# Performance work log

Measured on AMD Instinct MI355X. Metric: run time of the kernel, lower is better.

Reference implementation:

```python
import jax, jax.numpy as jnp
import numpy as np

B, S, D = 4, 2048, 1024
H, DK, DV = 16, 64, 64
SCALE = 8.0  # scaling_factor = sqrt(dk)


def setup_inputs() -> dict:
    key = jax.random.key(0)
    ks = jax.random.split(key, 9)
    s = 1.0 / np.sqrt(D)
    return {
        "q": jax.random.normal(ks[0], (B, S, D), jnp.float32),
        "k": jax.random.normal(ks[1], (B, S, D), jnp.float32),
        "v": jax.random.normal(ks[2], (B, S, D), jnp.float32),
        "Wq": jax.random.uniform(ks[3], (D, H * DK), jnp.float32, -s, s),
        "bq": jax.random.uniform(ks[4], (H * DK,), jnp.float32, -s, s),
        "Wk": jax.random.uniform(ks[5], (D, H * DK), jnp.float32, -s, s),
        "bk": jax.random.uniform(ks[6], (H * DK,), jnp.float32, -s, s),
        "Wv": jax.random.uniform(ks[7], (D, H * DV), jnp.float32, -s, s),
        "bv": jax.random.uniform(ks[8], (H * DV,), jnp.float32, -s, s),
    }


def reference(q, k, v, Wq, bq, Wk, bk, Wv, bv):
    # Linear projections, then split heads: [B,S,H*d] -> [B,S,H,d]
    qh = (q @ Wq + bq).reshape(B, S, H, DK)
    kh = (k @ Wk + bk).reshape(B, S, H, DK)
    vh = (v @ Wv + bv).reshape(B, S, H, DV)
    # scores: [B,H,Sq,Sk]
    e = jnp.einsum("bqhd,bkhd->bhqk", qh, kh) / SCALE
    attn = jax.nn.softmax(e, axis=-1)
    out = jnp.einsum("bhqk,bkhd->bqhd", attn, vh)  # [B,Sq,H,DV]
    return out.reshape(B, S, H * DV)  # dropout p=0 -> identity
```

## Files before the change

kernel.cpp:

```cpp
#include <hip/hip_runtime.h>
#include <hip/hip_bf16.h>


typedef unsigned short u16;
typedef unsigned int   u32;
typedef short bf16x8 __attribute__((ext_vector_type(8)));
typedef short bf16x4 __attribute__((ext_vector_type(4)));
typedef float f32x4  __attribute__((ext_vector_type(4)));
typedef u32   u32x4  __attribute__((ext_vector_type(4)));

#define S_TOT 2048
#define HD    1024
#define QK_SCALE 0.18033688f

#if __has_builtin(__builtin_amdgcn_exp2f)
#define EXP2(x) __builtin_amdgcn_exp2f(x)
#else
#define EXP2(x) exp2f(x)
#endif

__device__ __forceinline__ u16 f2bf(float f) {
  union { float f; unsigned u; } v; v.f = f;
  unsigned r = v.u + 0x7FFFu + ((v.u >> 16) & 1u);
  return (u16)(r >> 16);
}

__device__ __forceinline__ u32 cvt_pk_bf16(float lo, float hi) {
  u32 r;
  asm("v_cvt_pk_bf16_f32 %0, %1, %2" : "=v"(r) : "v"(lo), "v"(hi));
  return r;
}

__device__ __forceinline__ bf16x4 ds_tr16(unsigned a) {
  bf16x4 d;
  asm volatile("ds_read_b64_tr_b16 %0, %1" : "=v"(d) : "v"(a) : "memory");
  return d;
}

__device__ __forceinline__ void gld16(const u16* g, u16* l) {
  __builtin_amdgcn_global_load_lds(
      (const __attribute__((address_space(1))) u32*)g,
      (__attribute__((address_space(3))) u32*)l, 16, 0, 0);
}

#define LGKM_FENCE() do { asm volatile("s_waitcnt lgkmcnt(0)" ::: "memory"); \
                          __builtin_amdgcn_sched_barrier(0); } while (0)

#define PIPE_BAR(N) do { asm volatile("s_waitcnt vmcnt(" #N ")" ::: "memory"); \
                         __builtin_amdgcn_s_barrier(); \
                         __builtin_amdgcn_sched_barrier(0); } while (0)

__global__ __launch_bounds__(256)
void conv_kernel(const float* __restrict__ x0, const float* __restrict__ x1, const float* __restrict__ x2,
                 const float* __restrict__ w0, const float* __restrict__ w1, const float* __restrict__ w2,
                 u16* __restrict__ Xb, u16* __restrict__ Wt)
{
  const int z = blockIdx.y;
  const int t = threadIdx.x;
  if (blockIdx.x < 1024) {
    const float* X = z == 0 ? x0 : (z == 1 ? x1 : x2);
    u16* Xz = Xb + (size_t)z * 8388608;
    int tid = blockIdx.x * 256 + t;
#pragma unroll
    for (int i = 0; i < 8; ++i) {
      int c = tid + i * 262144;
      int row = c >> 8, k4 = (c & 255) * 4;
      const float4 xv = *(const float4*)&X[(size_t)row * 1024 + k4];
      int p = (k4 & ~31) + 8 * ((k4 & 15) >> 2) + 4 * ((k4 >> 4) & 1);
      p ^= (row & 6) << 2;
      bf16x4 sv = { (short)f2bf(xv.x), (short)f2bf(xv.y), (short)f2bf(xv.z), (short)f2bf(xv.w) };
      *(bf16x4*)&Xz[(size_t)row * 1024 + p] = sv;
    }
  } else {
    const float* W = z == 0 ? w0 : (z == 1 ? w1 : w2);
    u16* Wz = Wt + (size_t)z * 1048576;
    int tid = (blockIdx.x - 1024) * 256 + t;
#pragma unroll
    for (int i = 0; i < 8; ++i) {
      int c = tid + i * 32768;
      int n = c & 1023, k4 = (c >> 10) * 4;
      float wv0 = W[(size_t)(k4 + 0) * 1024 + n];
      float wv1 = W[(size_t)(k4 + 1) * 1024 + n];
      float wv2 = W[(size_t)(k4 + 2) * 1024 + n];
      float wv3 = W[(size_t)(k4 + 3) * 1024 + n];
      int kl = k4 & 31;
      int kp = 8 * ((kl & 15) >> 2) + 4 * ((kl >> 4) & 1);
      int off = ((n >> 7) * 32 + (k4 >> 5)) * 4096 + (n & 127) * 32
              + (kp ^ ((n & 6) << 2));
      bf16x4 sv = { (short)f2bf(wv0), (short)f2bf(wv1), (short)f2bf(wv2), (short)f2bf(wv3) };
      *(bf16x4*)&Wz[off] = sv;
    }
  }
}

__global__ __launch_bounds__(256)
void gemm_kernel(const u16* __restrict__ Xb, const u16* __restrict__ Wt,
                 const float* __restrict__ b0, const float* __restrict__ b1, const float* __restrict__ b2,
                 u16* __restrict__ o0, u16* __restrict__ o1, u16* __restrict__ vT)
{
  int p  = blockIdx.x + 8 * blockIdx.y + 512 * blockIdx.z;
  int wk = (p & 7) * 192 + (p >> 3);
  int nb = wk & 7, mb = (wk >> 3) & 63, z = wk >> 9;

  const u16* Xz = Xb + (size_t)z * 8388608;
  const u16* Wz = Wt + (size_t)z * 1048576;
  const float* BS = z == 0 ? b0 : (z == 1 ? b1 : b2);
  const float  osc = (z == 0) ? QK_SCALE : 1.0f;

  const int t = threadIdx.x;
  const int lane = t & 63, wid = t >> 6;
  const int g = lane >> 4, ln = lane & 15;
  const int mbase = mb * 128, nbase = nb * 128;
  const int xr = (ln & 6) << 2;

  __shared__ __align__(16) u16 Al[3][128 * 32];
  __shared__ __align__(16) u16 Bl[3][128 * 32];

  f32x4 acc[4][4];
#pragma unroll
  for (int i = 0; i < 4; ++i)
#pragma unroll
    for (int j = 0; j < 4; ++j) { acc[i][j][0]=0.f; acc[i][j][1]=0.f; acc[i][j][2]=0.f; acc[i][j][3]=0.f; }

  const u16* sa = Xz + (size_t)(mbase + (t >> 2)) * 1024 + (t & 3) * 8;
  const u16* sb = Wz + (size_t)(nb * 32) * 4096 + t * 8;
  u16* alw[3] = { &Al[0][wid * 512], &Al[1][wid * 512], &Al[2][wid * 512] };
  u16* blw[3] = { &Bl[0][wid * 512], &Bl[1][wid * 512], &Bl[2][wid * 512] };

  auto stage = [&](int kb, int buf) __attribute__((always_inline)) {
    gld16(sa + kb * 32,               alw[buf]);
    gld16(sa + kb * 32 + 64 * 1024,   alw[buf] + 2048);
    gld16(sb + kb * 4096,             blw[buf]);
    gld16(sb + kb * 4096 + 2048,      blw[buf] + 2048);
  };

  stage(0, 0);
  stage(1, 1);
  PIPE_BAR(4);

  if (z < 2) {
    const int wm = wid >> 1, wn = wid & 1;
    u16* O = z == 0 ? o0 : o1;

    auto compute = [&](int cur) __attribute__((always_inline)) {
      bf16x8 af[4], bfv[4];
#pragma unroll
      for (int mf = 0; mf < 4; ++mf)
        af[mf] = *(const bf16x8*)&Al[cur][(wm * 64 + mf * 16 + ln) * 32 + (g * 8 ^ xr)];
#pragma unroll
      for (int nf = 0; nf < 4; ++nf)
        bfv[nf] = *(const bf16x8*)&Bl[cur][(wn * 64 + nf * 16 + ln) * 32 + (g * 8 ^ xr)];
      __builtin_amdgcn_s_setprio(1);
#pragma unroll
      for (int mf = 0; mf < 4; ++mf)
#pragma unroll
        for (int nf = 0; nf < 4; ++nf)
          acc[mf][nf] = __builtin_amdgcn_mfma_f32_16x16x32_bf16(af[mf], bfv[nf], acc[mf][nf], 0, 0, 0);
      __builtin_amdgcn_s_setprio(0);
    };

    for (int kb = 0; kb < 30; kb += 3) {
      stage(kb + 2, 2); compute(0); PIPE_BAR(4);
      stage(kb + 3, 0); compute(1); PIPE_BAR(4);
      stage(kb + 4, 1); compute(2); PIPE_BAR(4);
    }
    compute(0); PIPE_BAR(0);
    compute(1);

#pragma unroll
    for (int nf = 0; nf < 4; ++nf) {
      int n = nbase + wn * 64 + nf * 16 + ln;
      float bv = BS[n];
#pragma unroll
      for (int mf = 0; mf < 4; ++mf)
#pragma unroll
        for (int r = 0; r < 4; ++r) {
          int m = mbase + wm * 64 + mf * 16 + 4 * g + r;
          O[(size_t)m * 1024 + n] = f2bf((acc[mf][nf][r] + bv) * osc);
        }
    }
  } else {
    const int wseq = wid >> 1, wdv = wid & 1;

    auto compute2 = [&](int cur) __attribute__((always_inline)) {
      bf16x8 afw[4], bfx[4];
#pragma unroll
      for (int mf = 0; mf < 4; ++mf)
        afw[mf] = *(const bf16x8*)&Bl[cur][(wdv * 64 + mf * 16 + ln) * 32 + (g * 8 ^ xr)];
#pragma unroll
      for (int nf = 0; nf < 4; ++nf)
        bfx[nf] = *(const bf16x8*)&Al[cur][(wseq * 64 + nf * 16 + ln) * 32 + (g * 8 ^ xr)];
      __builtin_amdgcn_s_setprio(1);
#pragma unroll
      for (int mf = 0; mf < 4; ++mf)
#pragma unroll
        for (int nf = 0; nf < 4; ++nf)
          acc[mf][nf] = __builtin_amdgcn_mfma_f32_16x16x32_bf16(afw[mf], bfx[nf], acc[mf][nf], 0, 0, 0);
      __builtin_amdgcn_s_setprio(0);
    };

    for (int kb = 0; kb < 30; kb += 3) {
      stage(kb + 2, 2); compute2(0); PIPE_BAR(4);
      stage(kb + 3, 0); compute2(1); PIPE_BAR(4);
      stage(kb + 4, 1); compute2(2); PIPE_BAR(4);
    }
    compute2(0); PIPE_BAR(0);
    compute2(1);

#pragma unroll
    for (int mf = 0; mf < 4; ++mf)
#pragma unroll
      for (int r = 0; r < 4; ++r) {
        int dvg = nbase + wdv * 64 + mf * 16 + 4 * g + r;
        float bv = BS[dvg];
        int hh = dvg >> 6, dvl = dvg & 63;
#pragma unroll
        for (int nf = 0; nf < 4; ++nf) {
          int m = mbase + wseq * 64 + nf * 16 + ln;
          int bb = m >> 11, ss = m & 2047;
          vT[((size_t)(bb * 16 + hh) * 64 + dvl) * 2048 + ss] = f2bf(acc[mf][nf][r] + bv);
        }
      }
  }
}

__global__ __launch_bounds__(256)
void proj_kernel(const float* __restrict__ x0, const float* __restrict__ x1, const float* __restrict__ x2,
                 const float* __restrict__ w0, const float* __restrict__ w1, const float* __restrict__ w2,
                 const float* __restrict__ b0, const float* __restrict__ b1, const float* __restrict__ b2,
                 u16* __restrict__ o0, u16* __restrict__ o1, u16* __restrict__ vT)
{
  int p  = blockIdx.x + 8 * blockIdx.y + 512 * blockIdx.z;
  int wk = (p & 7) * 192 + (p >> 3);
  int nb = wk & 7, mb = (wk >> 3) & 63, z = wk >> 9;

  const float* X  = z == 0 ? x0 : (z == 1 ? x1 : x2);
  const float* W  = z == 0 ? w0 : (z == 1 ? w1 : w2);
  const float* BS = z == 0 ? b0 : (z == 1 ? b1 : b2);
  const float  osc = (z == 0) ? QK_SCALE : 1.0f;

  const int t = threadIdx.x;
  const int lane = t & 63, wid = t >> 6;
  const int g = lane >> 4, ln = lane & 15;
  const int wm = wid >> 1, wn = wid & 1;
  const int mbase = mb * 128, nbase = nb * 128;

  __shared__ __align__(16) u16 As[128 * 40];
  __shared__ __align__(16) u16 Bs[16 * 272];

  f32x4 acc[4][4];
#pragma unroll
  for (int i = 0; i < 4; ++i)
#pragma unroll
    for (int j = 0; j < 4; ++j) { acc[i][j][0]=0.f; acc[i][j][1]=0.f; acc[i][j][2]=0.f; acc[i][j][3]=0.f; }

  const int arow = t >> 3;
  const int ak0  = (t & 7) * 4;
  const int ap   = 8 * ((ak0 & 15) >> 2) + 4 * (ak0 >> 4);
  const int bkr  = t >> 5;
  const int bnc  = (t & 31) * 4;
  const int bnblk = bnc >> 4, bncl = bnc & 15;

  const unsigned bs_base = (unsigned)(size_t)&Bs[0];

  for (int kb = 0; kb < 32; ++kb) {
    const int kbase = kb * 32;
#pragma unroll
    for (int ps = 0; ps < 4; ++ps) {
      int row = arow + 32 * ps;
      const float4 xv = *(const float4*)&X[(size_t)(mbase + row) * 1024 + kbase + ak0];
      bf16x4 sv = { (short)f2bf(xv.x), (short)f2bf(xv.y), (short)f2bf(xv.z), (short)f2bf(xv.w) };
      *(bf16x4*)&As[row * 40 + ap] = sv;
    }
#pragma unroll
    for (int ps = 0; ps < 4; ++ps) {
      int kr = bkr + 8 * ps;
      const float4 wv = *(const float4*)&W[(size_t)(kbase + kr) * 1024 + nbase + bnc];
      bf16x4 sv = { (short)f2bf(wv.x), (short)f2bf(wv.y), (short)f2bf(wv.z), (short)f2bf(wv.w) };
      *(bf16x4*)&Bs[(bnblk * 2 + (kr >> 4)) * 272 + (kr & 15) * 16 + bncl] = sv;
    }
    __syncthreads();

    bf16x8 af[4];
#pragma unroll
    for (int mf = 0; mf < 4; ++mf)
      af[mf] = *(const bf16x8*)&As[(wm * 64 + mf * 16 + ln) * 40 + g * 8];

    bf16x8 bfv[4];
#pragma unroll
    for (int nf = 0; nf < 4; ++nf) {
      unsigned base = bs_base + (unsigned)(((wn * 4 + nf) * 2) * 544) + lane * 8;
      bf16x4 lo = ds_tr16(base);
      bf16x4 hi = ds_tr16(base + 544);
      bf16x8 bb;
      bb[0]=lo[0]; bb[1]=lo[1]; bb[2]=lo[2]; bb[3]=lo[3];
      bb[4]=hi[0]; bb[5]=hi[1]; bb[6]=hi[2]; bb[7]=hi[3];
      bfv[nf] = bb;
    }
    LGKM_FENCE();
#pragma unroll
    for (int mf = 0; mf < 4; ++mf)
#pragma unroll
      for (int nf = 0; nf < 4; ++nf)
        acc[mf][nf] = __builtin_amdgcn_mfma_f32_16x16x32_bf16(af[mf], bfv[nf], acc[mf][nf], 0, 0, 0);
    __syncthreads();
  }

#pragma unroll
  for (int nf = 0; nf < 4; ++nf) {
    int n = nbase + wn * 64 + nf * 16 + ln;
    float bv = BS[n];
#pragma unroll
    for (int mf = 0; mf < 4; ++mf)
#pragma unroll
      for (int r = 0; r < 4; ++r) {
        int m = mbase + wm * 64 + mf * 16 + 4 * g + r;
        float val = (acc[mf][nf][r] + bv) * osc;
        if (z < 2) {
          u16* O = z == 0 ? o0 : o1;
          O[(size_t)m * 1024 + n] = f2bf(val);
        } else {
          vT[((size_t)((m >> 11) * 16 + (n >> 6)) * 64 + (n & 63)) * 2048 + (m & 2047)] = f2bf(val);
        }
      }
  }
}

__global__ __launch_bounds__(512)
void attn_kernel(const u16* __restrict__ qh, const u16* __restrict__ kh, const u16* __restrict__ vT,
                 float* __restrict__ out)
{
  int p  = blockIdx.x + 8 * blockIdx.y + 128 * blockIdx.z;
  int wk = (p & 7) * 64 + (p >> 3);
  int qt = wk & 7, h = (wk >> 3) & 15, b = wk >> 7;

  const int t = threadIdx.x;
  const int lane = t & 63, wid = t >> 6;
  const int g = lane >> 4, ln = lane & 15;
  const size_t bS = (size_t)b * S_TOT;
  const int qwin = qt * 256 + wid * 32;

  __shared__ __align__(16) u16 Ks[64 * 72];
  __shared__ __align__(16) u16 Vt[64 * 72];

  bf16x8 qf[2][2];
#pragma unroll
  for (int nf = 0; nf < 2; ++nf) {
    const u16* qrow = &qh[(bS + qwin + nf * 16 + ln) * HD + h * 64];
#pragma unroll
    for (int kk = 0; kk < 2; ++kk) {
      bf16x4 lo = *(const bf16x4*)&qrow[kk * 32 + 4 * g];
      bf16x4 hi = *(const bf16x4*)&qrow[kk * 32 + 4 * g + 16];
      bf16x8 qq;
      qq[0]=lo[0]; qq[1]=lo[1]; qq[2]=lo[2]; qq[3]=lo[3];
      qq[4]=hi[0]; qq[5]=hi[1]; qq[6]=hi[2]; qq[7]=hi[3];
      qf[nf][kk] = qq;
    }
  }

  bf16x8 ones;
#pragma unroll
  for (int j = 0; j < 8; ++j) ones[j] = (short)0x3F80;

  f32x4 o[2][4];
#pragma unroll
  for (int i = 0; i < 2; ++i)
#pragma unroll
    for (int j = 0; j < 4; ++j) { o[i][j][0]=0.f; o[i][j][1]=0.f; o[i][j][2]=0.f; o[i][j][3]=0.f; }
  f32x4 o1[2];
  o1[0][0]=0.f; o1[0][1]=0.f; o1[0][2]=0.f; o1[0][3]=0.f;
  o1[1][0]=0.f; o1[1][1]=0.f; o1[1][2]=0.f; o1[1][3]=0.f;

  const int skv = t >> 4;
  const int sd0 = (t & 15) * 4;
  const int kpos = 32 * (sd0 >> 5) + 8 * ((sd0 & 15) >> 2) + 4 * ((sd0 >> 4) & 1);
  u16* ksw[2];
  ksw[0] = &Ks[skv * 72 + kpos];
  ksw[1] = &Ks[(skv + 32) * 72 + kpos];
  const u16* kp = &kh[(bS + skv) * HD + h * 64 + sd0];

  const int vdv  = t >> 3;
  const int vkv8 = (t & 7) * 8;
  const int vp0  = 32 * (vkv8 >> 5) + 8 * ((vkv8 & 15) >> 2) + 4 * ((vkv8 >> 4) & 1);
  const int vkv4 = vkv8 + 4;
  const int vp1  = 32 * (vkv4 >> 5) + 8 * ((vkv4 & 15) >> 2) + 4 * ((vkv4 >> 4) & 1);
  u16* vsw0 = &Vt[vdv * 72 + vp0];
  u16* vsw1 = &Vt[vdv * 72 + vp1];
  const u16* vp = &vT[((size_t)(b * 16 + h) * 64 + vdv) * 2048 + vkv8];

  const size_t KSTEP = (size_t)64 * HD, C32 = (size_t)32 * HD;

  bf16x4 kr[2];
  kr[0] = *(const bf16x4*)kp; kr[1] = *(const bf16x4*)(kp + C32);
  bf16x8 vr = *(const bf16x8*)vp;
  kp += KSTEP; vp += 64;

  for (int it = 0; it < 32; ++it) {
    *(bf16x4*)ksw[0] = kr[0];
    *(bf16x4*)ksw[1] = kr[1];
    bf16x4 vlo = { vr[0], vr[1], vr[2], vr[3] };
    bf16x4 vhi = { vr[4], vr[5], vr[6], vr[7] };
    *(bf16x4*)vsw0 = vlo;
    *(bf16x4*)vsw1 = vhi;
    __syncthreads();

    if (it < 31) {
      kr[0] = *(const bf16x4*)kp; kr[1] = *(const bf16x4*)(kp + C32);
      vr = *(const bf16x8*)vp;
      kp += KSTEP; vp += 64;
    }

#pragma unroll
    for (int s = 0; s < 2; ++s) {
      bf16x8 kf[2][2];
#pragma unroll
      for (int mf = 0; mf < 2; ++mf)
#pragma unroll
        for (int kk = 0; kk < 2; ++kk)
          kf[mf][kk] = *(const bf16x8*)&Ks[(s * 32 + mf * 16 + ln) * 72 + kk * 32 + 8 * g];

      f32x4 sc[2][2];
      __builtin_amdgcn_s_setprio(1);
#pragma unroll
      for (int mf = 0; mf < 2; ++mf)
#pragma unroll
        for (int nf = 0; nf < 2; ++nf) {
          f32x4 a; a[0]=0.f; a[1]=0.f; a[2]=0.f; a[3]=0.f;
#pragma unroll
          for (int kk = 0; kk < 2; ++kk)
            a = __builtin_amdgcn_mfma_f32_16x16x32_bf16(kf[mf][kk], qf[nf][kk], a, 0, 0, 0);
          sc[mf][nf] = a;
        }
      __builtin_amdgcn_s_setprio(0);

      bf16x8 vf[4];
#pragma unroll
      for (int nf = 0; nf < 4; ++nf)
        vf[nf] = *(const bf16x8*)&Vt[(nf * 16 + ln) * 72 + s * 32 + 8 * g];

      bf16x8 pa[2];
#pragma unroll
      for (int nf = 0; nf < 2; ++nf) {
        float pv[2][4];
#pragma unroll
        for (int mf = 0; mf < 2; ++mf)
#pragma unroll
          for (int r = 0; r < 4; ++r)
            pv[mf][r] = EXP2(sc[mf][nf][r]);
        union { u32x4 u; bf16x8 b; } pk;
        pk.u[0] = cvt_pk_bf16(pv[0][0], pv[0][1]);
        pk.u[1] = cvt_pk_bf16(pv[0][2], pv[0][3]);
        pk.u[2] = cvt_pk_bf16(pv[1][0], pv[1][1]);
        pk.u[3] = cvt_pk_bf16(pv[1][2], pv[1][3]);
        pa[nf] = pk.b;
      }

      __builtin_amdgcn_s_setprio(1);
#pragma unroll
      for (int mq = 0; mq < 2; ++mq) {
#pragma unroll
        for (int nf = 0; nf < 4; ++nf)
          o[mq][nf] = __builtin_amdgcn_mfma_f32_16x16x32_bf16(pa[mq], vf[nf], o[mq][nf], 0, 0, 0);
        o1[mq] = __builtin_amdgcn_mfma_f32_16x16x32_bf16(pa[mq], ones, o1[mq], 0, 0, 0);
      }
      __builtin_amdgcn_s_setprio(0);
    }
    __syncthreads();
  }

#pragma unroll
  for (int mq = 0; mq < 2; ++mq)
#pragma unroll
    for (int r = 0; r < 4; ++r) {
      float inv = 1.0f / o1[mq][r];
      int qrow = qwin + mq * 16 + 4 * g + r;
#pragma unroll
      for (int nf = 0; nf < 4; ++nf)
        out[(bS + qrow) * HD + h * 64 + nf * 16 + ln] = o[mq][nf][r] * inv;
    }
}

extern "C" void kernel_launch(void* const* d_in, const int* in_sizes, int n_in,
                              void* d_out, int out_size, void* d_ws, size_t ws_size,
                              hipStream_t stream) {
  const float* q  = (const float*)d_in[0];
  const float* k  = (const float*)d_in[1];
  const float* v  = (const float*)d_in[2];
  const float* Wq = (const float*)d_in[3];
  const float* bq = (const float*)d_in[4];
  const float* Wk = (const float*)d_in[5];
  const float* bk = (const float*)d_in[6];
  const float* Wv = (const float*)d_in[7];
  const float* bv = (const float*)d_in[8];
  float* out = (float*)d_out;

  u16* qh = (u16*)d_ws;
  u16* kh = qh + (size_t)8192 * 1024;
  u16* vT = kh + (size_t)8192 * 1024;

  const size_t XB_OFF = (size_t)3 * 8192 * 1024;
  const size_t WT_OFF = XB_OFF + (size_t)3 * 8192 * 1024;
  const size_t NEED   = (WT_OFF + (size_t)3 * 1024 * 1024) * 2;

  if (ws_size >= NEED) {
    u16* Xb = (u16*)d_ws + XB_OFF;
    u16* Wt = (u16*)d_ws + WT_OFF;
    conv_kernel<<<dim3(1152, 3), 256, 0, stream>>>(q, k, v, Wq, Wk, Wv, Xb, Wt);
    gemm_kernel<<<dim3(8, 64, 3), 256, 0, stream>>>(Xb, Wt, bq, bk, bv, qh, kh, vT);
  } else {
    proj_kernel<<<dim3(8, 64, 3), 256, 0, stream>>>(q, k, v, Wq, Wk, Wv, bq, bk, bv, qh, kh, vT);
  }
  attn_kernel<<<dim3(8, 16, 4), 512, 0, stream>>>(qh, kh, vT, out);
}
```

Before: 171.0 us.

## Load weight fragments directly from global into registers, bypassing LDS

The pre-packed bf16 weight tile is now read straight from global memory into MFMA operand registers, with register double-buffering across k-steps, instead of being staged through shared memory. The repack layout drops the XOR swizzle because the LDS bank-conflict avoidance no longer applies. This halves LDS traffic and footprint per block, which may raise occupancy. The cost is more global/L2 reads, since each wave pair re-reads the same weight fragments, and register pressure goes up; the pipeline wait counts are adjusted to match.

```diff
diff --git a/kernel.cpp b/kernel.cpp
--- a/kernel.cpp
+++ b/kernel.cpp
@@ -85,8 +85,7 @@
       float wv3 = W[(size_t)(k4 + 3) * 1024 + n];
       int kl = k4 & 31;
       int kp = 8 * ((kl & 15) >> 2) + 4 * ((kl >> 4) & 1);
-      int off = ((n >> 7) * 32 + (k4 >> 5)) * 4096 + (n & 127) * 32
-              + (kp ^ ((n & 6) << 2));
+      int off = ((n >> 7) * 32 + (k4 >> 5)) * 4096 + (n & 127) * 32 + kp;
       bf16x4 sv = { (short)f2bf(wv0), (short)f2bf(wv1), (short)f2bf(wv2), (short)f2bf(wv3) };
       *(bf16x4*)&Wz[off] = sv;
     }
@@ -114,7 +113,6 @@
   const int xr = (ln & 6) << 2;
 
   __shared__ __align__(16) u16 Al[3][128 * 32];
-  __shared__ __align__(16) u16 Bl[3][128 * 32];
 
   f32x4 acc[4][4];
 #pragma unroll
@@ -123,53 +121,62 @@
     for (int j = 0; j < 4; ++j) { acc[i][j][0]=0.f; acc[i][j][1]=0.f; acc[i][j][2]=0.f; acc[i][j][3]=0.f; }
 
   const u16* sa = Xz + (size_t)(mbase + (t >> 2)) * 1024 + (t & 3) * 8;
-  const u16* sb = Wz + (size_t)(nb * 32) * 4096 + t * 8;
   u16* alw[3] = { &Al[0][wid * 512], &Al[1][wid * 512], &Al[2][wid * 512] };
-  u16* blw[3] = { &Bl[0][wid * 512], &Bl[1][wid * 512], &Bl[2][wid * 512] };
 
   auto stage = [&](int kb, int buf) __attribute__((always_inline)) {
     gld16(sa + kb * 32,               alw[buf]);
     gld16(sa + kb * 32 + 64 * 1024,   alw[buf] + 2048);
-    gld16(sb + kb * 4096,             blw[buf]);
-    gld16(sb + kb * 4096 + 2048,      blw[buf] + 2048);
   };
 
+  const int whalf = (z < 2) ? (wid & 1) : (wid & 1);
+  const u16* wfp = Wz + (size_t)(nb * 32) * 4096
+                 + (whalf * 64 + ln) * 32 + g * 8;
+
+  auto loadB = [&](int kb, bf16x8* dst) __attribute__((always_inline)) {
+#pragma unroll
+    for (int nf = 0; nf < 4; ++nf)
+      dst[nf] = *(const bf16x8*)(wfp + (size_t)kb * 4096 + nf * 512);
+  };
+
+  bf16x8 bA[4], bB[4];
+
   stage(0, 0);
+  loadB(0, bA);
   stage(1, 1);
-  PIPE_BAR(4);
+  PIPE_BAR(6);
 
   if (z < 2) {
-    const int wm = wid >> 1, wn = wid & 1;
+    const int wm = wid >> 1;
     u16* O = z == 0 ? o0 : o1;
 
-    auto compute = [&](int cur) __attribute__((always_inline)) {
-      bf16x8 af[4], bfv[4];
+    auto compute = [&](int cur, const bf16x8* bq) __attribute__((always_inline)) {
+      bf16x8 af[4];
 #pragma unroll
       for (int mf = 0; mf < 4; ++mf)
         af[mf] = *(const bf16x8*)&Al[cur][(wm * 64 + mf * 16 + ln) * 32 + (g * 8 ^ xr)];
-#pragma unroll
-      for (int nf = 0; nf < 4; ++nf)
-        bfv[nf] = *(const bf16x8*)&Bl[cur][(wn * 64 + nf * 16 + ln) * 32 + (g * 8 ^ xr)];
       __builtin_amdgcn_s_setprio(1);
 #pragma unroll
       for (int mf = 0; mf < 4; ++mf)
 #pragma unroll
         for (int nf = 0; nf < 4; ++nf)
-          acc[mf][nf] = __builtin_amdgcn_mfma_f32_16x16x32_bf16(af[mf], bfv[nf], acc[mf][nf], 0, 0, 0);
+          acc[mf][nf] = __builtin_amdgcn_mfma_f32_16x16x32_bf16(af[mf], bq[nf], acc[mf][nf], 0, 0, 0);
       __builtin_amdgcn_s_setprio(0);
     };
 
-    for (int kb = 0; kb < 30; kb += 3) {
-      stage(kb + 2, 2); compute(0); PIPE_BAR(4);
-      stage(kb + 3, 0); compute(1); PIPE_BAR(4);
-      stage(kb + 4, 1); compute(2); PIPE_BAR(4);
-    }
-    compute(0); PIPE_BAR(0);
-    compute(1);
+    for (int kb = 0; kb < 30; kb += 6) {
+      stage(kb + 2, 2); loadB(kb + 1, bB); compute(0, bA); PIPE_BAR(6);
+      stage(kb + 3, 0); loadB(kb + 2, bA); compute(1, bB); PIPE_BAR(6);
+      stage(kb + 4, 1); loadB(kb + 3, bB); compute(2, bA); PIPE_BAR(6);
+      stage(kb + 5, 2); loadB(kb + 4, bA); compute(0, bB); PIPE_BAR(6);
+      stage(kb + 6, 0); loadB(kb + 5, bB); compute(1, bA); PIPE_BAR(6);
+      stage(kb + 7, 1); loadB(kb + 6, bA); compute(2, bB); PIPE_BAR(6);
+    }
+    loadB(31, bB); compute(0, bA); PIPE_BAR(0);
+    compute(1, bB);
 
 #pragma unroll
     for (int nf = 0; nf < 4; ++nf) {
-      int n = nbase + wn * 64 + nf * 16 + ln;
+      int n = nbase + whalf * 64 + nf * 16 + ln;
       float bv = BS[n];
 #pragma unroll
       for (int mf = 0; mf < 4; ++mf)
@@ -180,13 +187,10 @@
         }
     }
   } else {
-    const int wseq = wid >> 1, wdv = wid & 1;
-
-    auto compute2 = [&](int cur) __attribute__((always_inline)) {
-      bf16x8 afw[4], bfx[4];
-#pragma unroll
-      for (int mf = 0; mf < 4; ++mf)
-        afw[mf] = *(const bf16x8*)&Bl[cur][(wdv * 64 + mf * 16 + ln) * 32 + (g * 8 ^ xr)];
+    const int wseq = wid >> 1;
+
+    auto compute2 = [&](int cur, const bf16x8* wq) __attribute__((always_inline)) {
+      bf16x8 bfx[4];
 #pragma unroll
       for (int nf = 0; nf < 4; ++nf)
         bfx[nf] = *(const bf16x8*)&Al[cur][(wseq * 64 + nf * 16 + ln) * 32 + (g * 8 ^ xr)];
@@ -195,23 +199,26 @@
       for (int mf = 0; mf < 4; ++mf)
 #pragma unroll
         for (int nf = 0; nf < 4; ++nf)
-          acc[mf][nf] = __builtin_amdgcn_mfma_f32_16x16x32_bf16(afw[mf], bfx[nf], acc[mf][nf], 0, 0, 0);
+          acc[mf][nf] = __builtin_amdgcn_mfma_f32_16x16x32_bf16(wq[mf], bfx[nf], acc[mf][nf], 0, 0, 0);
       __builtin_amdgcn_s_setprio(0);
     };
 
-    for (int kb = 0; kb < 30; kb += 3) {
-      stage(kb + 2, 2); compute2(0); PIPE_BAR(4);
-      stage(kb + 3, 0); compute2(1); PIPE_BAR(4);
-      stage(kb + 4, 1); compute2(2); PIPE_BAR(4);
-    }
-    compute2(0); PIPE_BAR(0);
-    compute2(1);
+    for (int kb = 0; kb < 30; kb += 6) {
+      stage(kb + 2, 2); loadB(kb + 1, bB); compute2(0, bA); PIPE_BAR(6);
+      stage(kb + 3, 0); loadB(kb + 2, bA); compute2(1, bB); PIPE_BAR(6);
+      stage(kb + 4, 1); loadB(kb + 3, bB); compute2(2, bA); PIPE_BAR(6);
+      stage(kb + 5, 2); loadB(kb + 4, bA); compute2(0, bB); PIPE_BAR(6);
+      stage(kb + 6, 0); loadB(kb + 5, bB); compute2(1, bA); PIPE_BAR(6);
+      stage(kb + 7, 1); loadB(kb + 6, bA); compute2(2, bB); PIPE_BAR(6);
+    }
+    loadB(31, bB); compute2(0, bA); PIPE_BAR(0);
+    compute2(1, bB);
 
 #pragma unroll
     for (int mf = 0; mf < 4; ++mf)
 #pragma unroll
       for (int r = 0; r < 4; ++r) {
-        int dvg = nbase + wdv * 64 + mf * 16 + 4 * g + r;
+        int dvg = nbase + whalf * 64 + mf * 16 + 4 * g + r;
         float bv = BS[dvg];
         int hh = dvg >> 6, dvl = dvg & 63;
 #pragma unroll
```

Result: no change. 168.6 us (-1.4%).
